# Optimization experiments

Measured on AMD Instinct MI355X. Metric: run time of the kernel, lower is better.

## Reference

```python
import jax, jax.numpy as jnp
import numpy as np

# hyperparameters (from init_kwargs)
GAMMA = 2.0
KEEP_WEIGHT = 1.0
T_TEMP = 0.07
M = 0.5
COS_M = float(np.cos(M))
SIN_M = float(np.sin(M))
THRESHOLD = float(np.cos(np.pi - M))
MM = float(np.sin(np.pi - M) * M)
ALPHA = 0.1
T_BUF0 = 0.0  # registered buffer t initialized to zero
VALID_THRESHOLD = 0.8
EPS = 1e-12  # F.normalize eps


def setup_inputs() -> dict:
    key = jax.random.key(0)
    k1, k2, k3 = jax.random.split(key, 3)
    N, C = 8192, 128
    return {
        "feature1": jax.random.normal(k1, (N, C), jnp.float32),
        "feature2": jax.random.normal(k2, (N, C), jnp.float32),
        "labels": jax.random.randint(k3, (N,), 0, 1024, dtype=jnp.int32),
    }


def reference(feature1, feature2, labels):
    N = feature1.shape[0]
    f1 = feature1 / jnp.maximum(jnp.linalg.norm(feature1, axis=1, keepdims=True), EPS)
    f2 = feature2 / jnp.maximum(jnp.linalg.norm(feature2, axis=1, keepdims=True), EPS)

    # [N, N] similarity, clamped to [-1, 1]
    sim = jnp.clip(jnp.einsum('nc,kc->nk', f1, f2), -1.0, 1.0)

    pos = (labels[:, None] == labels[None, :]).astype(sim.dtype)  # [N, N]
    neg = 1.0 - pos
    pos_mask = pos > 0

    # buffer update t (no_grad in original)
    mean_ts = jax.lax.stop_gradient((sim * pos).sum() / pos.sum())
    t = ALPHA * mean_ts + (1.0 - ALPHA) * T_BUF0
    weight_valid = t > VALID_THRESHOLD

    # curricular margin on positive entries
    sin_theta = jnp.sqrt(1.0 - sim * sim)
    cos_theta_m = sim * COS_M - sin_theta * SIN_M
    final_pos = jnp.where(sim > THRESHOLD, cos_theta_m, sim - MM)
    sim2 = jnp.where(pos_mask, final_pos, sim)

    # per-row mean of (margined) positive similarities
    row_target = (sim2 * pos).sum(axis=1) / pos.sum(axis=1)  # [N]
    hard_mask = sim2 > row_target[:, None]
    sim3 = jnp.where(hard_mask, sim2 * (t + sim2), sim2)
    sim4 = jnp.where(pos_mask, final_pos, sim3)

    logits = jnp.exp(sim4 / T_TEMP)

    # focal-style reweighting (only used when weight_valid)
    diff_pos = (pos - sim * pos) ** GAMMA + KEEP_WEIGHT * pos
    diff_neg = jnp.clip(sim * neg, 0.0, 1.0) ** GAMMA + KEEP_WEIGHT * neg

    logit_pos = jnp.where(weight_valid, (logits * diff_pos).sum(axis=1), (logits * pos).sum(axis=1))
    logit_neg = jnp.where(weight_valid, (logits * diff_neg).sum(axis=1), (logits * neg).sum(axis=1))

    loss = -jnp.log(logit_pos / (logit_neg + logit_pos)).sum() / N
    return loss
```

## Files before the change

### kernel.cpp

```cpp
#include <hip/hip_runtime.h>

#define N_ROWS 8192
#define N_LBL  1024

constexpr float C_COS_M  = (float)0.8775825618903728;
constexpr float C_SIN_M  = (float)0.479425538604203;
constexpr float C_THRESH = (float)-0.8775825618903728;
constexpr float C_MM     = (float)0.2397127693021015;
constexpr float C_ALPHA  = 0.1f;
constexpr float C_VALID  = 0.8f;
constexpr float C_K2E    = (float)(1.0 / (0.07 * 0.6931471805599453));
constexpr float C_LN2    = 0.6931471805599453f;

typedef short s16x8 __attribute__((ext_vector_type(8)));
typedef float f32x4 __attribute__((ext_vector_type(4)));

__device__ __forceinline__ unsigned f2bf(float f) {
    unsigned u = __float_as_uint(f);
    return (u + 0x7fffu + ((u >> 16) & 1u)) >> 16;
}
__device__ __forceinline__ float bflo(unsigned u) { return __uint_as_float(u << 16); }
__device__ __forceinline__ float bfhi(unsigned u) { return __uint_as_float(u & 0xffff0000u); }

__device__ __forceinline__ void gl_lds16(const unsigned* g, void* lds) {
    __builtin_amdgcn_global_load_lds(
        (const __attribute__((address_space(1))) unsigned*)g,
        (__attribute__((address_space(3))) unsigned*)lds, 16, 0, 0);
}

__global__ void k_norm_hist(const float* __restrict__ f1, const float* __restrict__ f2,
                            const int* __restrict__ labels,
                            unsigned* __restrict__ f1n, unsigned* __restrict__ f2n,
                            int* __restrict__ hist) {
    int b = blockIdx.x * 4 + (threadIdx.x >> 6);
    int l = threadIdx.x & 63;
    int row = (b < N_ROWS) ? b : (b - N_ROWS);
    const float* src = (b < N_ROWS) ? f1 : f2;
    unsigned* dst = (b < N_ROWS) ? f1n : f2n;
    float2 v = ((const float2*)(src + row * 128))[l];
    float ss = v.x * v.x + v.y * v.y;
    #pragma unroll
    for (int k = 1; k < 64; k <<= 1) ss += __shfl_xor(ss, k);
    float inv = 1.0f / fmaxf(sqrtf(ss), 1e-12f);
    dst[row * 64 + l] = f2bf(v.x * inv) | (f2bf(v.y * inv) << 16);
    if (b < N_ROWS && l == 0) atomicAdd(&hist[labels[row]], 1);
}

__global__ void k_scan_scatter(const int* __restrict__ hist, const int* __restrict__ labels,
                               int* __restrict__ offs, unsigned short* __restrict__ bucket) {
    __shared__ int loffs[N_LBL];
    __shared__ int wsum[16];
    int t = threadIdx.x, lane = t & 63, w = t >> 6;
    int v = hist[t];
    int x = v;
    #pragma unroll
    for (int k = 1; k < 64; k <<= 1) {
        int n = __shfl_up(x, k);
        if (lane >= k) x += n;
    }
    if (lane == 63) wsum[w] = x;
    __syncthreads();
    if (t < 16) {
        int own = wsum[t];
        int y = own;
        #pragma unroll
        for (int k = 1; k < 16; k <<= 1) {
            int n = __shfl_up(y, k);
            if (t >= k) y += n;
        }
        wsum[t] = y - own;
    }
    __syncthreads();
    int excl = x - v + wsum[w];
    loffs[t] = excl;
    offs[t] = excl;
    __syncthreads();
    for (int j = t; j < N_ROWS; j += 1024) {
        int p = atomicAdd(&loffs[labels[j]], 1);
        bucket[p] = (unsigned short)j;
    }
}

__global__ void k_passA(const unsigned* __restrict__ f1n, const unsigned* __restrict__ f2n,
                        const int* __restrict__ labels, const int* __restrict__ hist,
                        const int* __restrict__ offs, const unsigned short* __restrict__ bucket,
                        float* __restrict__ rt, float* __restrict__ row_sim,
                        float* __restrict__ simlist) {
    int i = blockIdx.x, lane = threadIdx.x;
    int g = lane >> 4, sl = lane & 15;
    uint4 a = ((const uint4*)(f1n + i * 64))[sl];
    float a0 = bflo(a.x), a1 = bfhi(a.x), a2 = bflo(a.y), a3 = bfhi(a.y);
    float a4 = bflo(a.z), a5 = bfhi(a.z), a6 = bflo(a.w), a7 = bfhi(a.w);
    int lab = labels[i];
    int cnt = hist[lab], st = offs[lab];
    float rs_sim = 0.f, rs_fp = 0.f;
    for (int e0 = 0; e0 < cnt; e0 += 4) {
        int e = e0 + g;
        bool val = e < cnt;
        int j = bucket[st + (val ? e : 0)];
        uint4 b = ((const uint4*)(f2n + j * 64))[sl];
        float p = a0 * bflo(b.x) + a1 * bfhi(b.x) + a2 * bflo(b.y) + a3 * bfhi(b.y)
                + a4 * bflo(b.z) + a5 * bfhi(b.z) + a6 * bflo(b.w) + a7 * bfhi(b.w);
        p += __shfl_xor(p, 1);
        p += __shfl_xor(p, 2);
        p += __shfl_xor(p, 4);
        p += __shfl_xor(p, 8);
        float s = fminf(1.f, fmaxf(-1.f, p));
        float ctm = s * C_COS_M - sqrtf(fmaxf(0.f, 1.f - s * s)) * C_SIN_M;
        float fpv = (s > C_THRESH) ? ctm : (s - C_MM);
        if (val) {
            rs_sim += s;
            rs_fp += fpv;
            if (sl == 0) simlist[i * 128 + e] = s;
        }
    }
    rs_sim += __shfl_xor(rs_sim, 16); rs_sim += __shfl_xor(rs_sim, 32);
    rs_fp  += __shfl_xor(rs_fp, 16);  rs_fp  += __shfl_xor(rs_fp, 32);
    if (lane == 0) { rt[i] = rs_fp / (float)cnt; row_sim[i] = rs_sim; }
}

__global__ void k_finalize(const float* __restrict__ row_sim, const int* __restrict__ hist,
                           float* __restrict__ tw) {
    int t = threadIdx.x;
    float ssum = 0.f, scnt = 0.f;
    for (int l = t; l < N_LBL; l += 256) {
        float h = (float)hist[l];
        scnt += h * h;
    }
    for (int i = t; i < N_ROWS; i += 256) ssum += row_sim[i];
    #pragma unroll
    for (int k = 1; k < 64; k <<= 1) {
        ssum += __shfl_xor(ssum, k);
        scnt += __shfl_xor(scnt, k);
    }
    __shared__ float sa[4], sb[4];
    if ((t & 63) == 0) { sa[t >> 6] = ssum; sb[t >> 6] = scnt; }
    __syncthreads();
    if (t == 0) {
        float tv = C_ALPHA * ((sa[0] + sa[1] + sa[2] + sa[3]) / (sb[0] + sb[1] + sb[2] + sb[3]));
        tw[0] = tv;
        tw[1] = (tv > C_VALID) ? 1.f : 0.f;
    }
}

template <bool WV>
__device__ __forceinline__ void epi_accum(const f32x4 (&acc)[4][4], const float (&rtv)[4][4],
                                          float (&lnp)[4][4], float tval) {
    #pragma unroll
    for (int mt = 0; mt < 4; ++mt)
        #pragma unroll
        for (int nt = 0; nt < 4; ++nt)
            #pragma unroll
            for (int r = 0; r < 4; ++r) {
                float s = acc[mt][nt][r];
                float u = C_K2E * s;
                float v = u * (tval + s);
                float arg = (s > rtv[mt][r]) ? v : u;
                float e = __builtin_amdgcn_exp2f(arg);
                if (WV) { float cz = fminf(fmaxf(s, 0.f), 1.f); e *= cz * cz + 1.f; }
                lnp[mt][r] += e;
            }
}

__global__ __launch_bounds__(256, 2) void k_passB(const unsigned* __restrict__ f1n,
                                                  const unsigned* __restrict__ f2n,
                                                  const float* __restrict__ rt,
                                                  const float* __restrict__ tw,
                                                  float* __restrict__ lnacc) {
    __shared__ __align__(16) unsigned char ldsA[32768];
    __shared__ __align__(16) unsigned char ldsB[32768];
    const int tid = threadIdx.x;
    const int wave = tid >> 6, lane = tid & 63;
    const int wr = wave >> 1, wc = wave & 1;
    const int quad = lane >> 4, l15 = lane & 15;
    const int rowbase = blockIdx.x * 128;
    const float tval = tw[0];
    const bool wv = (tw[1] != 0.f);

    const int srow = tid >> 4;
    const int sq   = (tid & 15) ^ (srow & 15);
    const int goff = srow * 64 + sq * 4;
    const int loff = wave * 1024;

    {
        const unsigned* gA = f1n + rowbase * 64 + goff;
        const unsigned* gB = f2n + (blockIdx.y * 512) * 64 + goff;
        #pragma unroll
        for (int it = 0; it < 8; ++it) {
            gl_lds16(gA + it * 1024, ldsA + loff + it * 4096);
            gl_lds16(gB + it * 1024, ldsB + loff + it * 4096);
        }
    }

    float rtv[4][4];
    #pragma unroll
    for (int mt = 0; mt < 4; ++mt)
        #pragma unroll
        for (int r = 0; r < 4; ++r)
            rtv[mt][r] = rt[rowbase + wr * 64 + mt * 16 + quad * 4 + r];

    __syncthreads();

    float lnp[4][4] = {};
    #pragma unroll
    for (int ctile = 0; ctile < 4; ++ctile) {
        f32x4 zero = {0.f, 0.f, 0.f, 0.f};
        f32x4 acc[4][4];
        #pragma unroll
        for (int mt = 0; mt < 4; ++mt)
            #pragma unroll
            for (int nt = 0; nt < 4; ++nt) acc[mt][nt] = zero;

        #pragma unroll
        for (int ks = 0; ks < 4; ++ks) {
            s16x8 af[4], bfr[4];
            #pragma unroll
            for (int mt = 0; mt < 4; ++mt) {
                int row = wr * 64 + mt * 16 + l15, q = ks * 4 + quad;
                af[mt] = *((const s16x8*)(ldsA + row * 256 + ((q ^ (row & 15)) << 4)));
            }
            #pragma unroll
            for (int nt = 0; nt < 4; ++nt) {
                int row = wc * 64 + nt * 16 + l15, q = ks * 4 + quad;
                bfr[nt] = *((const s16x8*)(ldsB + row * 256 + ((q ^ (row & 15)) << 4)));
            }
            #pragma unroll
            for (int mt = 0; mt < 4; ++mt)
                #pragma unroll
                for (int nt = 0; nt < 4; ++nt)
                    acc[mt][nt] = __builtin_amdgcn_mfma_f32_16x16x32_bf16(af[mt], bfr[nt],
                                                                          acc[mt][nt], 0, 0, 0);
        }

        __syncthreads();
        if (ctile < 3) {
            const unsigned* gB = f2n + (blockIdx.y * 512 + (ctile + 1) * 128) * 64 + goff;
            #pragma unroll
            for (int it = 0; it < 8; ++it)
                gl_lds16(gB + it * 1024, ldsB + loff + it * 4096);
        }

        if (wv) epi_accum<true>(acc, rtv, lnp, tval);
        else    epi_accum<false>(acc, rtv, lnp, tval);

        if (ctile < 3) __syncthreads();
    }

    #pragma unroll
    for (int mt = 0; mt < 4; ++mt)
        #pragma unroll
        for (int r = 0; r < 4; ++r) {
            float v = lnp[mt][r];
            v += __shfl_xor(v, 1);
            v += __shfl_xor(v, 2);
            v += __shfl_xor(v, 4);
            v += __shfl_xor(v, 8);
            if (l15 == 0)
                atomicAdd(&lnacc[rowbase + wr * 64 + mt * 16 + quad * 4 + r], v);
        }
}

__global__ void k_lossC(const float* __restrict__ simlist, const int* __restrict__ labels,
                        const int* __restrict__ hist, const float* __restrict__ rt,
                        const float* __restrict__ tw, const float* __restrict__ lnacc,
                        float* __restrict__ out) {
    int t = threadIdx.x;
    int sub = t >> 3, sl = t & 7;
    int i = blockIdx.x * 32 + sub;
    int cnt = hist[labels[i]];
    if (cnt > 128) cnt = 128;
    float tval = tw[0];
    bool wv = (tw[1] != 0.f);
    float rti = rt[i];
    float lp = 0.f, den = 0.f;
    for (int e = sl; e < cnt; e += 8) {
        float s = simlist[i * 128 + e];
        float sh = (s > rti) ? s * (tval + s) : s;
        float en = __builtin_amdgcn_exp2f(C_K2E * sh);
        float ctm = s * C_COS_M - sqrtf(fmaxf(0.f, 1.f - s * s)) * C_SIN_M;
        float fp = (s > C_THRESH) ? ctm : (s - C_MM);
        float ep = __builtin_amdgcn_exp2f(C_K2E * fp);
        if (wv) {
            float cz = fminf(fmaxf(s, 0.f), 1.f);
            en *= cz * cz + 1.f;
            float d = 1.f - s;
            ep *= d * d + 1.f;
        }
        den -= en;
        lp += ep;
    }
    #pragma unroll
    for (int k = 1; k < 8; k <<= 1) {
        den += __shfl_xor(den, k);
        lp += __shfl_xor(lp, k);
    }
    float ln = lnacc[i] + den;
    float rl = (__builtin_amdgcn_logf(lp + ln) - __builtin_amdgcn_logf(lp)) * C_LN2;
    rl += __shfl_xor(rl, 8);
    rl += __shfl_xor(rl, 16);
    rl += __shfl_xor(rl, 32);
    __shared__ float sa[4];
    if ((t & 63) == 0) sa[t >> 6] = rl;
    __syncthreads();
    if (t == 0)
        atomicAdd(out, (sa[0] + sa[1] + sa[2] + sa[3]) * (1.0f / (float)N_ROWS));
}

extern "C" void kernel_launch(void* const* d_in, const int* in_sizes, int n_in,
                              void* d_out, int out_size, void* d_ws, size_t ws_size,
                              hipStream_t stream) {
    (void)in_sizes; (void)n_in; (void)out_size; (void)ws_size;
    const float* f1 = (const float*)d_in[0];
    const float* f2 = (const float*)d_in[1];
    const int* labels = (const int*)d_in[2];
    float* out = (float*)d_out;
    char* ws = (char*)d_ws;

    unsigned* f1n          = (unsigned*)(ws + 0);
    unsigned* f2n          = (unsigned*)(ws + 2097152);
    float* simlist         = (float*)(ws + 4194304);
    float* row_sim         = (float*)(ws + 8388608);
    float* rt              = (float*)(ws + 8421376);
    int* offs              = (int*)(ws + 8454144);
    unsigned short* bucket = (unsigned short*)(ws + 8458240);
    float* tw              = (float*)(ws + 8474624);
    float* lnacc           = (float*)(ws + 8474688);
    int* hist              = (int*)(ws + 8507456);

    hipMemsetAsync(ws + 8474688, 0, 36864, stream);
    hipMemsetAsync(out, 0, 4, stream);

    k_norm_hist<<<dim3(4096), dim3(256), 0, stream>>>(f1, f2, labels, f1n, f2n, hist);
    k_scan_scatter<<<dim3(1), dim3(1024), 0, stream>>>(hist, labels, offs, bucket);
    k_passA<<<dim3(N_ROWS), dim3(64), 0, stream>>>(f1n, f2n, labels, hist, offs, bucket,
                                                   rt, row_sim, simlist);
    k_finalize<<<dim3(1), dim3(256), 0, stream>>>(row_sim, hist, tw);
    k_passB<<<dim3(64, 16), dim3(256), 0, stream>>>(f1n, f2n, rt, tw, lnacc);
    k_lossC<<<dim3(256), dim3(256), 0, stream>>>(simlist, labels, hist, rt, tw, lnacc, out);
}
```

Before: 128.4 us.

## Collapse label bucketing into per-label pair kernel and retile similarity pass

```diff
diff --git a/kernel.cpp b/kernel.cpp
--- a/kernel.cpp
+++ b/kernel.cpp
@@ -2,6 +2,7 @@
 
 #define N_ROWS 8192
 #define N_LBL  1024
+#define KMAX   64
 
 constexpr float C_COS_M  = (float)0.8775825618903728;
 constexpr float C_SIN_M  = (float)0.479425538604203;
@@ -28,10 +29,10 @@
         (__attribute__((address_space(3))) unsigned*)lds, 16, 0, 0);
 }
 
-__global__ void k_norm_hist(const float* __restrict__ f1, const float* __restrict__ f2,
-                            const int* __restrict__ labels,
-                            unsigned* __restrict__ f1n, unsigned* __restrict__ f2n,
-                            int* __restrict__ hist) {
+__global__ void k_norm(const float* __restrict__ f1, const float* __restrict__ f2,
+                       unsigned* __restrict__ f1n, unsigned* __restrict__ f2n,
+                       float* __restrict__ gsum) {
+    if (blockIdx.x == 0 && threadIdx.x == 0) { gsum[0] = 0.f; gsum[1] = 0.f; }
     int b = blockIdx.x * 4 + (threadIdx.x >> 6);
     int l = threadIdx.x & 63;
     int row = (b < N_ROWS) ? b : (b - N_ROWS);
@@ -43,139 +44,113 @@
     for (int k = 1; k < 64; k <<= 1) ss += __shfl_xor(ss, k);
     float inv = 1.0f / fmaxf(sqrtf(ss), 1e-12f);
     dst[row * 64 + l] = f2bf(v.x * inv) | (f2bf(v.y * inv) << 16);
-    if (b < N_ROWS && l == 0) atomicAdd(&hist[labels[row]], 1);
-}
-
-__global__ void k_scan_scatter(const int* __restrict__ hist, const int* __restrict__ labels,
-                               int* __restrict__ offs, unsigned short* __restrict__ bucket) {
-    __shared__ int loffs[N_LBL];
-    __shared__ int wsum[16];
-    int t = threadIdx.x, lane = t & 63, w = t >> 6;
-    int v = hist[t];
-    int x = v;
-    #pragma unroll
-    for (int k = 1; k < 64; k <<= 1) {
-        int n = __shfl_up(x, k);
-        if (lane >= k) x += n;
-    }
-    if (lane == 63) wsum[w] = x;
+}
+
+__global__ __launch_bounds__(64) void k_pairs(const unsigned* __restrict__ f1n,
+                                              const unsigned* __restrict__ f2n,
+                                              const int* __restrict__ labels,
+                                              float* __restrict__ simlist,
+                                              float* __restrict__ rt,
+                                              int* __restrict__ rowcnt,
+                                              float* __restrict__ gsum,
+                                              float* __restrict__ out) {
+    __shared__ int members[KMAX];
+    __shared__ unsigned ldsF1[KMAX * 64];
+    __shared__ unsigned ldsF2[KMAX * 64];
+    const int lab = blockIdx.x, lane = threadIdx.x;
+    if (lab == 0 && lane == 0) out[0] = 0.f;
+
+    int base = 0;
+    #pragma unroll 2
+    for (int c = 0; c < 128; ++c) {
+        int lv = labels[c * 64 + lane];
+        unsigned long long m = __ballot(lv == lab);
+        if (lv == lab) {
+            int idx = base + __popcll(m & ((1ull << lane) - 1ull));
+            if (idx < KMAX) members[idx] = c * 64 + lane;
+        }
+        base += (int)__popcll(m);
+    }
+    int k = base < KMAX ? base : KMAX;
     __syncthreads();
-    if (t < 16) {
-        int own = wsum[t];
-        int y = own;
-        #pragma unroll
-        for (int k = 1; k < 16; k <<= 1) {
-            int n = __shfl_up(y, k);
-            if (t >= k) y += n;
-        }
-        wsum[t] = y - own;
+    if (k == 0) return;
+
+    for (int m = 0; m < k; ++m) {
+        int r = members[m];
+        ldsF1[m * 64 + lane] = f1n[r * 64 + lane];
+        ldsF2[m * 64 + lane] = f2n[r * 64 + lane];
+        if (lane == 0) rowcnt[r] = k;
     }
     __syncthreads();
-    int excl = x - v + wsum[w];
-    loffs[t] = excl;
-    offs[t] = excl;
-    __syncthreads();
-    for (int j = t; j < N_ROWS; j += 1024) {
-        int p = atomicAdd(&loffs[labels[j]], 1);
-        bucket[p] = (unsigned short)j;
-    }
-}
-
-__global__ void k_passA(const unsigned* __restrict__ f1n, const unsigned* __restrict__ f2n,
-                        const int* __restrict__ labels, const int* __restrict__ hist,
-                        const int* __restrict__ offs, const unsigned short* __restrict__ bucket,
-                        float* __restrict__ rt, float* __restrict__ row_sim,
-                        float* __restrict__ simlist) {
-    int i = blockIdx.x, lane = threadIdx.x;
-    int g = lane >> 4, sl = lane & 15;
-    uint4 a = ((const uint4*)(f1n + i * 64))[sl];
-    float a0 = bflo(a.x), a1 = bfhi(a.x), a2 = bflo(a.y), a3 = bfhi(a.y);
-    float a4 = bflo(a.z), a5 = bfhi(a.z), a6 = bflo(a.w), a7 = bfhi(a.w);
-    int lab = labels[i];
-    int cnt = hist[lab], st = offs[lab];
-    float rs_sim = 0.f, rs_fp = 0.f;
-    for (int e0 = 0; e0 < cnt; e0 += 4) {
-        int e = e0 + g;
-        bool val = e < cnt;
-        int j = bucket[st + (val ? e : 0)];
-        uint4 b = ((const uint4*)(f2n + j * 64))[sl];
-        float p = a0 * bflo(b.x) + a1 * bfhi(b.x) + a2 * bflo(b.y) + a3 * bfhi(b.y)
-                + a4 * bflo(b.z) + a5 * bfhi(b.z) + a6 * bflo(b.w) + a7 * bfhi(b.w);
-        p += __shfl_xor(p, 1);
-        p += __shfl_xor(p, 2);
-        p += __shfl_xor(p, 4);
-        p += __shfl_xor(p, 8);
-        float s = fminf(1.f, fmaxf(-1.f, p));
-        float ctm = s * C_COS_M - sqrtf(fmaxf(0.f, 1.f - s * s)) * C_SIN_M;
-        float fpv = (s > C_THRESH) ? ctm : (s - C_MM);
-        if (val) {
-            rs_sim += s;
-            rs_fp += fpv;
-            if (sl == 0) simlist[i * 128 + e] = s;
-        }
-    }
-    rs_sim += __shfl_xor(rs_sim, 16); rs_sim += __shfl_xor(rs_sim, 32);
-    rs_fp  += __shfl_xor(rs_fp, 16);  rs_fp  += __shfl_xor(rs_fp, 32);
-    if (lane == 0) { rt[i] = rs_fp / (float)cnt; row_sim[i] = rs_sim; }
-}
-
-__global__ void k_finalize(const float* __restrict__ row_sim, const int* __restrict__ hist,
-                           float* __restrict__ tw) {
-    int t = threadIdx.x;
-    float ssum = 0.f, scnt = 0.f;
-    for (int l = t; l < N_LBL; l += 256) {
-        float h = (float)hist[l];
-        scnt += h * h;
-    }
-    for (int i = t; i < N_ROWS; i += 256) ssum += row_sim[i];
-    #pragma unroll
-    for (int k = 1; k < 64; k <<= 1) {
-        ssum += __shfl_xor(ssum, k);
-        scnt += __shfl_xor(scnt, k);
-    }
-    __shared__ float sa[4], sb[4];
-    if ((t & 63) == 0) { sa[t >> 6] = ssum; sb[t >> 6] = scnt; }
-    __syncthreads();
-    if (t == 0) {
-        float tv = C_ALPHA * ((sa[0] + sa[1] + sa[2] + sa[3]) / (sb[0] + sb[1] + sb[2] + sb[3]));
-        tw[0] = tv;
-        tw[1] = (tv > C_VALID) ? 1.f : 0.f;
+
+    const int g = lane >> 4, sl = lane & 15;
+    float bsim = 0.f;
+    for (int mi = 0; mi < k; ++mi) {
+        const int ri = members[mi];
+        uint4 a = ((const uint4*)(ldsF1 + mi * 64))[sl];
+        float a0 = bflo(a.x), a1 = bfhi(a.x), a2 = bflo(a.y), a3 = bfhi(a.y);
+        float a4 = bflo(a.z), a5 = bfhi(a.z), a6 = bflo(a.w), a7 = bfhi(a.w);
+        float accfp = 0.f;
+        for (int mj = g; mj < k; mj += 4) {
+            uint4 bb = ((const uint4*)(ldsF2 + mj * 64))[sl];
+            float p = a0 * bflo(bb.x) + a1 * bfhi(bb.x) + a2 * bflo(bb.y) + a3 * bfhi(bb.y)
+                    + a4 * bflo(bb.z) + a5 * bfhi(bb.z) + a6 * bflo(bb.w) + a7 * bfhi(bb.w);
+            p += __shfl_xor(p, 1);
+            p += __shfl_xor(p, 2);
+            p += __shfl_xor(p, 4);
+            p += __shfl_xor(p, 8);
+            float s = fminf(1.f, fmaxf(-1.f, p));
+            float ctm = s * C_COS_M - sqrtf(fmaxf(0.f, 1.f - s * s)) * C_SIN_M;
+            float fpv = (s > C_THRESH) ? ctm : (s - C_MM);
+            if (sl == 0) simlist[ri * 64 + mj] = s;
+            accfp += fpv;
+            bsim += s;
+        }
+        accfp += __shfl_xor(accfp, 16);
+        accfp += __shfl_xor(accfp, 32);
+        if (lane == 0) rt[ri] = accfp / (float)k;
+    }
+    bsim += __shfl_xor(bsim, 16);
+    bsim += __shfl_xor(bsim, 32);
+    if (lane == 0) {
+        atomicAdd(&gsum[0], bsim);
+        atomicAdd(&gsum[1], (float)(k * k));
     }
 }
 
 template <bool WV>
-__device__ __forceinline__ void epi_accum(const f32x4 (&acc)[4][4], const float (&rtv)[4][4],
+__device__ __forceinline__ void epi_accum(const f32x4 (&acc)[4][2], const float (&rtv)[4][4],
                                           float (&lnp)[4][4], float tval) {
     #pragma unroll
     for (int mt = 0; mt < 4; ++mt)
         #pragma unroll
-        for (int nt = 0; nt < 4; ++nt)
+        for (int nt = 0; nt < 2; ++nt)
             #pragma unroll
             for (int r = 0; r < 4; ++r) {
                 float s = acc[mt][nt][r];
                 float u = C_K2E * s;
-                float v = u * (tval + s);
-                float arg = (s > rtv[mt][r]) ? v : u;
+                float m = tval + s;
+                float arg = (s > rtv[mt][r]) ? u * m : u;
                 float e = __builtin_amdgcn_exp2f(arg);
-                if (WV) { float cz = fminf(fmaxf(s, 0.f), 1.f); e *= cz * cz + 1.f; }
+                if (WV) { float cz = fmaxf(s, 0.f); e *= cz * cz + 1.f; }
                 lnp[mt][r] += e;
             }
 }
 
-__global__ __launch_bounds__(256, 2) void k_passB(const unsigned* __restrict__ f1n,
+__global__ __launch_bounds__(512, 4) void k_passB(const unsigned* __restrict__ f1n,
                                                   const unsigned* __restrict__ f2n,
                                                   const float* __restrict__ rt,
-                                                  const float* __restrict__ tw,
-                                                  float* __restrict__ lnacc) {
+                                                  const float* __restrict__ gsum,
+                                                  float* __restrict__ lnacc2) {
     __shared__ __align__(16) unsigned char ldsA[32768];
     __shared__ __align__(16) unsigned char ldsB[32768];
     const int tid = threadIdx.x;
     const int wave = tid >> 6, lane = tid & 63;
-    const int wr = wave >> 1, wc = wave & 1;
+    const int wr = wave >> 2, wc = wave & 3;
     const int quad = lane >> 4, l15 = lane & 15;
     const int rowbase = blockIdx.x * 128;
-    const float tval = tw[0];
-    const bool wv = (tw[1] != 0.f);
+    const float tval = C_ALPHA * gsum[0] / gsum[1];
+    const bool wv = (tval > C_VALID);
 
     const int srow = tid >> 4;
     const int sq   = (tid & 15) ^ (srow & 15);
@@ -184,11 +159,11 @@
 
     {
         const unsigned* gA = f1n + rowbase * 64 + goff;
-        const unsigned* gB = f2n + (blockIdx.y * 512) * 64 + goff;
-        #pragma unroll
-        for (int it = 0; it < 8; ++it) {
-            gl_lds16(gA + it * 1024, ldsA + loff + it * 4096);
-            gl_lds16(gB + it * 1024, ldsB + loff + it * 4096);
+        const unsigned* gB = f2n + (blockIdx.y * 1024) * 64 + goff;
+        #pragma unroll
+        for (int it = 0; it < 4; ++it) {
+            gl_lds16(gA + it * 2048, ldsA + loff + it * 8192);
+            gl_lds16(gB + it * 2048, ldsB + loff + it * 8192);
         }
     }
 
@@ -202,50 +177,51 @@
     __syncthreads();
 
     float lnp[4][4] = {};
-    #pragma unroll
-    for (int ctile = 0; ctile < 4; ++ctile) {
+    #pragma unroll 1
+    for (int ctile = 0; ctile < 8; ++ctile) {
         f32x4 zero = {0.f, 0.f, 0.f, 0.f};
-        f32x4 acc[4][4];
+        f32x4 acc[4][2];
         #pragma unroll
         for (int mt = 0; mt < 4; ++mt)
             #pragma unroll
-            for (int nt = 0; nt < 4; ++nt) acc[mt][nt] = zero;
+            for (int nt = 0; nt < 2; ++nt) acc[mt][nt] = zero;
 
         #pragma unroll
         for (int ks = 0; ks < 4; ++ks) {
-            s16x8 af[4], bfr[4];
+            s16x8 af[4], bfr[2];
             #pragma unroll
             for (int mt = 0; mt < 4; ++mt) {
                 int row = wr * 64 + mt * 16 + l15, q = ks * 4 + quad;
                 af[mt] = *((const s16x8*)(ldsA + row * 256 + ((q ^ (row & 15)) << 4)));
             }
             #pragma unroll
-            for (int nt = 0; nt < 4; ++nt) {
-                int row = wc * 64 + nt * 16 + l15, q = ks * 4 + quad;
+            for (int nt = 0; nt < 2; ++nt) {
+                int row = wc * 32 + nt * 16 + l15, q = ks * 4 + quad;
                 bfr[nt] = *((const s16x8*)(ldsB + row * 256 + ((q ^ (row & 15)) << 4)));
             }
             #pragma unroll
             for (int mt = 0; mt < 4; ++mt)
                 #pragma unroll
-                for (int nt = 0; nt < 4; ++nt)
+                for (int nt = 0; nt < 2; ++nt)
                     acc[mt][nt] = __builtin_amdgcn_mfma_f32_16x16x32_bf16(af[mt], bfr[nt],
                                                                           acc[mt][nt], 0, 0, 0);
         }
 
         __syncthreads();
-        if (ctile < 3) {
-            const unsigned* gB = f2n + (blockIdx.y * 512 + (ctile + 1) * 128) * 64 + goff;
-            #pragma unroll
-            for (int it = 0; it < 8; ++it)
-                gl_lds16(gB + it * 1024, ldsB + loff + it * 4096);
+        if (ctile < 7) {
+            const unsigned* gB = f2n + (blockIdx.y * 1024 + (ctile + 1) * 128) * 64 + goff;
+            #pragma unroll
+            for (int it = 0; it < 4; ++it)
+                gl_lds16(gB + it * 2048, ldsB + loff + it * 8192);
         }
 
         if (wv) epi_accum<true>(acc, rtv, lnp, tval);
         else    epi_accum<false>(acc, rtv, lnp, tval);
 
-        if (ctile < 3) __syncthreads();
-    }
-
+        if (ctile < 7) __syncthreads();
+    }
+
+    const int slice = blockIdx.y * 4 + wc;
     #pragma unroll
     for (int mt = 0; mt < 4; ++mt)
         #pragma unroll
@@ -256,32 +232,31 @@
             v += __shfl_xor(v, 4);
             v += __shfl_xor(v, 8);
             if (l15 == 0)
-                atomicAdd(&lnacc[rowbase + wr * 64 + mt * 16 + quad * 4 + r], v);
-        }
-}
-
-__global__ void k_lossC(const float* __restrict__ simlist, const int* __restrict__ labels,
-                        const int* __restrict__ hist, const float* __restrict__ rt,
-                        const float* __restrict__ tw, const float* __restrict__ lnacc,
-                        float* __restrict__ out) {
+                lnacc2[slice * N_ROWS + rowbase + wr * 64 + mt * 16 + quad * 4 + r] = v;
+        }
+}
+
+__global__ void k_lossC(const float* __restrict__ simlist, const int* __restrict__ rowcnt,
+                        const float* __restrict__ rt, const float* __restrict__ gsum,
+                        const float* __restrict__ lnacc2, float* __restrict__ out) {
     int t = threadIdx.x;
     int sub = t >> 3, sl = t & 7;
     int i = blockIdx.x * 32 + sub;
-    int cnt = hist[labels[i]];
-    if (cnt > 128) cnt = 128;
-    float tval = tw[0];
-    bool wv = (tw[1] != 0.f);
+    int cnt = rowcnt[i];
+    if (cnt > KMAX) cnt = KMAX;
+    float tval = C_ALPHA * gsum[0] / gsum[1];
+    bool wv = (tval > C_VALID);
     float rti = rt[i];
     float lp = 0.f, den = 0.f;
     for (int e = sl; e < cnt; e += 8) {
-        float s = simlist[i * 128 + e];
+        float s = simlist[i * 64 + e];
         float sh = (s > rti) ? s * (tval + s) : s;
         float en = __builtin_amdgcn_exp2f(C_K2E * sh);
         float ctm = s * C_COS_M - sqrtf(fmaxf(0.f, 1.f - s * s)) * C_SIN_M;
         float fp = (s > C_THRESH) ? ctm : (s - C_MM);
         float ep = __builtin_amdgcn_exp2f(C_K2E * fp);
         if (wv) {
-            float cz = fminf(fmaxf(s, 0.f), 1.f);
+            float cz = fmaxf(s, 0.f);
             en *= cz * cz + 1.f;
             float d = 1.f - s;
             ep *= d * d + 1.f;
@@ -289,12 +264,16 @@
         den -= en;
         lp += ep;
     }
+    float lnsum = 0.f;
+    #pragma unroll
+    for (int p = 0; p < 4; ++p) lnsum += lnacc2[(sl + p * 8) * N_ROWS + i];
     #pragma unroll
     for (int k = 1; k < 8; k <<= 1) {
         den += __shfl_xor(den, k);
         lp += __shfl_xor(lp, k);
-    }
-    float ln = lnacc[i] + den;
+        lnsum += __shfl_xor(lnsum, k);
+    }
+    float ln = lnsum + den;
     float rl = (__builtin_amdgcn_logf(lp + ln) - __builtin_amdgcn_logf(lp)) * C_LN2;
     rl += __shfl_xor(rl, 8);
     rl += __shfl_xor(rl, 16);
@@ -316,25 +295,17 @@
     float* out = (float*)d_out;
     char* ws = (char*)d_ws;
 
-    unsigned* f1n          = (unsigned*)(ws + 0);
-    unsigned* f2n          = (unsigned*)(ws + 2097152);
-    float* simlist         = (float*)(ws + 4194304);
-    float* row_sim         = (float*)(ws + 8388608);
-    float* rt              = (float*)(ws + 8421376);
-    int* offs              = (int*)(ws + 8454144);
-    unsigned short* bucket = (unsigned short*)(ws + 8458240);
-    float* tw              = (float*)(ws + 8474624);
-    float* lnacc           = (float*)(ws + 8474688);
-    int* hist              = (int*)(ws + 8507456);
-
-    hipMemsetAsync(ws + 8474688, 0, 36864, stream);
-    hipMemsetAsync(out, 0, 4, stream);
-
-    k_norm_hist<<<dim3(4096), dim3(256), 0, stream>>>(f1, f2, labels, f1n, f2n, hist);
-    k_scan_scatter<<<dim3(1), dim3(1024), 0, stream>>>(hist, labels, offs, bucket);
-    k_passA<<<dim3(N_ROWS), dim3(64), 0, stream>>>(f1n, f2n, labels, hist, offs, bucket,
-                                                   rt, row_sim, simlist);
-    k_finalize<<<dim3(1), dim3(256), 0, stream>>>(row_sim, hist, tw);
-    k_passB<<<dim3(64, 16), dim3(256), 0, stream>>>(f1n, f2n, rt, tw, lnacc);
-    k_lossC<<<dim3(256), dim3(256), 0, stream>>>(simlist, labels, hist, rt, tw, lnacc, out);
-}
+    unsigned* f1n   = (unsigned*)(ws + 0);
+    unsigned* f2n   = (unsigned*)(ws + 2097152);
+    float* simlist  = (float*)(ws + 4194304);
+    float* rt       = (float*)(ws + 6291456);
+    int* rowcnt     = (int*)(ws + 6324224);
+    float* lnacc2   = (float*)(ws + 6356992);
+    float* gsum     = (float*)(ws + 7405568);
+
+    k_norm<<<dim3(4096), dim3(256), 0, stream>>>(f1, f2, f1n, f2n, gsum);
+    k_pairs<<<dim3(N_LBL), dim3(64), 0, stream>>>(f1n, f2n, labels, simlist, rt, rowcnt,
+                                                  gsum, out);
+    k_passB<<<dim3(64, 8), dim3(512), 0, stream>>>(f1n, f2n, rt, gsum, lnacc2);
+    k_lossC<<<dim3(256), dim3(256), 0, stream>>>(simlist, rowcnt, rt, gsum, lnacc2, out);
+}
```

New measurement: 172.5 us. +34.4%, slower.
